# Kernel tuning notes

Hardware: AMD Instinct MI355X
Metric: run time of the kernel (lower is better)

The kernel has to match this reference:

```python
import jax, jax.numpy as jnp
import numpy as np

BN_EPS = 1e-5
K = 9  # 3x3 kernel positions


def conv2d(x, w, b, pad, dil=1):
    out = jax.lax.conv_general_dilated(
        x, w, window_strides=(1, 1), padding=((pad, pad), (pad, pad)),
        rhs_dilation=(dil, dil), dimension_numbers=('NCHW', 'OIHW', 'NCHW'))
    return out + b[None, :, None, None]


def bn_relu(x, g, be, mu, var):
    inv = jax.lax.rsqrt(var + BN_EPS)
    return jax.nn.relu((x - mu[None, :, None, None]) * (g * inv)[None, :, None, None] + be[None, :, None, None])


def deform_conv(x, w_om, b_om, w, b):
    # DCNv2-style modulated deformable 3x3 conv, stride 1, pad 1, dg=1.
    B, C, H, W = x.shape
    om = conv2d(x, w_om, b_om, pad=1)               # [B, 27, H, W]
    o1, o2, m = jnp.split(om, 3, axis=1)            # dy, dx, mask logits: [B,9,H,W]
    mask = jax.nn.sigmoid(m)
    ky, kx = jnp.meshgrid(jnp.arange(3), jnp.arange(3), indexing='ij')
    ky = (ky.reshape(-1) - 1).astype(x.dtype)       # kernel offsets in {-1,0,1}
    kx = (kx.reshape(-1) - 1).astype(x.dtype)
    py = jnp.arange(H, dtype=x.dtype)[None, None, :, None] + ky[None, :, None, None] + o1  # [B,9,H,W]
    px = jnp.arange(W, dtype=x.dtype)[None, None, None, :] + kx[None, :, None, None] + o2

    y0 = jnp.floor(py); x0 = jnp.floor(px)
    wy1 = py - y0; wx1 = px - x0
    y0i = y0.astype(jnp.int32); x0i = x0.astype(jnp.int32)
    x_flat = x.reshape(B, C, H * W)

    def corner(yi, xi, wgt):
        valid = ((yi >= 0) & (yi < H) & (xi >= 0) & (xi < W)).astype(x.dtype)
        idx = jnp.clip(yi, 0, H - 1) * W + jnp.clip(xi, 0, W - 1)      # [B,9,H,W]
        g = jax.vmap(lambda xf, i: xf[:, i])(x_flat, idx.reshape(B, -1))
        g = g.reshape(B, C, K, H, W)
        return g * (wgt * valid)[:, None]

    cols = (corner(y0i,     x0i,     (1 - wy1) * (1 - wx1))
            + corner(y0i,     x0i + 1, (1 - wy1) * wx1)
            + corner(y0i + 1, x0i,     wy1 * (1 - wx1))
            + corner(y0i + 1, x0i + 1, wy1 * wx1))                       # [B,C,9,H,W]
    cols = cols * mask[:, None]
    out = jnp.einsum('bckhw,ock->bohw', cols, w.reshape(w.shape[0], C, K))
    return out + b[None, :, None, None]


def setup_inputs() -> dict:
    key = jax.random.key(0)
    ks = jax.random.split(key, 24)
    B, C, H, W = 2, 64, 256, 256
    d = {}
    d['x'] = jax.random.normal(ks[0], (B, C, H, W), jnp.float32)
    d['w_om'] = jax.random.normal(ks[1], (27, C, 3, 3), jnp.float32) * 0.01
    d['b_om'] = jax.random.normal(ks[2], (27,), jnp.float32) * 0.01
    d['w_dcn'] = jax.random.normal(ks[3], (C, C, 3, 3), jnp.float32) * 0.05
    d['b_dcn'] = jax.random.normal(ks[4], (C,), jnp.float32) * 0.05
    for i, pfx in enumerate(['bn1', 'bn2', 'bn3']):
        d[pfx + '_g'] = jax.random.uniform(ks[5 + 4 * i], (C,), jnp.float32, 0.5, 1.5)
        d[pfx + '_b'] = jax.random.normal(ks[6 + 4 * i], (C,), jnp.float32) * 0.05
        d[pfx + '_m'] = jax.random.normal(ks[7 + 4 * i], (C,), jnp.float32) * 0.05
        d[pfx + '_v'] = jax.random.uniform(ks[8 + 4 * i], (C,), jnp.float32, 0.5, 1.5)
    d['w_h'] = jax.random.normal(ks[17], (C, C, 3, 3), jnp.float32) * 0.05
    d['b_h'] = jax.random.normal(ks[18], (C,), jnp.float32) * 0.05
    d['w_w'] = jax.random.normal(ks[19], (C, C, 3, 3), jnp.float32) * 0.05
    d['b_w'] = jax.random.normal(ks[20], (C,), jnp.float32) * 0.05
    d['w3'] = jax.random.normal(ks[21], (1, C, 3, 3), jnp.float32) * 0.05
    d['b3'] = jax.random.normal(ks[22], (1,), jnp.float32) * 0.05
    return d


def reference(x, w_om, b_om, w_dcn, b_dcn,
              bn1_g, bn1_b, bn1_m, bn1_v,
              w_h, b_h, bn2_g, bn2_b, bn2_m, bn2_v,
              w_w, b_w, bn3_g, bn3_b, bn3_m, bn3_v,
              w3, b3):
    h = deform_conv(x, w_om, b_om, w_dcn, b_dcn)
    h = bn_relu(h, bn1_g, bn1_b, bn1_m, bn1_v)
    h = conv2d(h, w_h, b_h, pad=2, dil=2)
    h = bn_relu(h, bn2_g, bn2_b, bn2_m, bn2_v)
    h = conv2d(h, w_w, b_w, pad=2, dil=2)
    h = bn_relu(h, bn3_g, bn3_b, bn3_m, bn3_v)
    h = conv2d(h, w3, b3, pad=1)
    return jnp.clip(jax.nn.sigmoid(h), 1e-4, 1.0 - 1e-4)
```

## Files before the change

kernel.cpp:

```cpp
#include <hip/hip_runtime.h>
#include <math.h>

#define HH 256
#define WW 256
#define HW (HH*WW)
#define NPX (2*HW)

typedef __attribute__((ext_vector_type(8))) short bf16x8;
typedef __attribute__((ext_vector_type(4))) float f32x4;

__device__ __forceinline__ float bf2f(short h) {
    union { unsigned u; float f; } v; v.u = ((unsigned)(unsigned short)h) << 16; return v.f;
}
__device__ __forceinline__ short f2bf(float f) {
    union { float f; unsigned u; } v; v.f = f;
    unsigned r = v.u + 0x7fffu + ((v.u >> 16) & 1u);
    return (short)(r >> 16);
}
__device__ __forceinline__ short f2bf_fast(float f) {
    union { float f; unsigned u; } v; v.f = f;
    return (short)((v.u + 0x8000u) >> 16);
}

__global__ __launch_bounds__(256) void k_prep_w(
        const float* __restrict__ w_om, const float* __restrict__ w_dcn,
        const float* __restrict__ w_h,  const float* __restrict__ w_w,
        const float* __restrict__ w3,
        short* __restrict__ wt_om, short* __restrict__ wt_dcn,
        short* __restrict__ wt_h,  short* __restrict__ wt_w,
        float* __restrict__ w3t) {
    int i = blockIdx.x * 256 + threadIdx.x;
    if (i >= 64 * 576) return;
    int o = i / 576, k = i - o * 576, t = k >> 6, c = k & 63;
    int kb = k >> 3, j = k & 7;
    int src = (o * 64 + c) * 9 + t;
    int dst = (kb * 64 + o) * 8 + j;
    wt_dcn[dst] = f2bf(w_dcn[src]);
    wt_h[dst]   = f2bf(w_h[src]);
    wt_w[dst]   = f2bf(w_w[src]);
    if (o < 32) wt_om[(kb * 32 + o) * 8 + j] = (o < 27) ? f2bf(w_om[src]) : (short)0;
    if (o == 0) w3t[k] = w3[c * 9 + t];
}

__global__ __launch_bounds__(256) void k_x2cl(const float* __restrict__ x,
        short* __restrict__ xcl) {
    __shared__ short tile[256 * 66];
    const int xx = threadIdx.x;
    const int row = blockIdx.x;
    const int b = row >> 8, y = row & 255;
    for (int c = 0; c < 64; ++c)
        tile[xx * 66 + c] = f2bf(x[((b * 64 + c) << 16) + (y << 8) + xx]);
    __syncthreads();
    short* op = xcl + ((row << 8) + xx) * 64;
#pragma unroll
    for (int j = 0; j < 8; ++j) {
        bf16x8 v;
#pragma unroll
        for (int e = 0; e < 8; ++e) v[e] = tile[xx * 66 + j * 8 + e];
        *(bf16x8*)(op + j * 8) = v;
    }
}

#define XPS 72

__global__ __launch_bounds__(256) __attribute__((amdgpu_waves_per_eu(2, 4)))
void k_dcn_mfma(const short* __restrict__ xcl,
        const short* __restrict__ wom, const float* __restrict__ b_om,
        const short* __restrict__ wt,
        const float* __restrict__ bias,
        const float* __restrict__ gg, const float* __restrict__ be,
        const float* __restrict__ mu, const float* __restrict__ var,
        short* __restrict__ out_cl) {
    __shared__ short xt[256 * XPS];
    __shared__ float om_lds[64 * 28];
    const int lane = threadIdx.x & 63, wave = threadIdx.x >> 6;
    const int quad = lane >> 4, l16 = lane & 15;
    const int band = blockIdx.x & 7, idx = blockIdx.x >> 3;
    const int tr = band * 8 + (idx >> 5), tc = idx & 31;
    const int b = tr >> 5;
    const int ty0 = (tr & 31) * 8, tx0 = tc * 8;
    const int base = b << 16;
    const int hy0 = ty0 - 4, hx0 = tx0 - 4;
    {
        const int p = threadIdx.x;
        const int sy = min(max(hy0 + (p >> 4), 0), 255);
        const int sx = min(max(hx0 + (p & 15), 0), 255);
        const short* src = xcl + (size_t)((base + sy * 256 + sx) * 64);
        short* dst = &xt[p * XPS];
#pragma unroll
        for (int j = 0; j < 8; ++j)
            *(bf16x8*)(dst + j * 8) = *(const bf16x8*)(src + j * 8);
    }
    __syncthreads();

    const int lp = wave * 16 + l16;
    const int pyy = lp >> 3, pxx = lp & 7;
    const int y = ty0 + pyy, x = tx0 + pxx;

    {
        f32x4 oacc[2];
        oacc[0] = (f32x4){0,0,0,0}; oacc[1] = (f32x4){0,0,0,0};
        auto loadOB = [&](int s, bf16x8* Bv) {
            const int kb = s * 4 + quad;
#pragma unroll
            for (int g = 0; g < 2; ++g)
                Bv[g] = *(const bf16x8*)(wom + (kb * 32 + g * 16 + l16) * 8);
        };
        bf16x8 OB[2][2];
        loadOB(0, OB[0]);
#pragma unroll
        for (int s = 0; s < 18; ++s) {
            if (s < 17) loadOB(s + 1, OB[(s + 1) & 1]);
            const int t = s >> 1, c0 = (s & 1) * 32;
            const int dy = t / 3 - 1, dx = t % 3 - 1;
            bf16x8 av = *(const bf16x8*)&xt[((pyy + 4 + dy) * 16 + (pxx + 4 + dx)) * XPS + c0 + quad * 8];
            bool ok = ((unsigned)(y + dy) < 256u) && ((unsigned)(x + dx) < 256u);
            if (!ok) { bf16x8 z = {0,0,0,0,0,0,0,0}; av = z; }
#pragma unroll
            for (int g = 0; g < 2; ++g)
                oacc[g] = __builtin_amdgcn_mfma_f32_16x16x32_bf16(av, OB[s & 1][g], oacc[g], 0, 0, 0);
        }
#pragma unroll
        for (int g = 0; g < 2; ++g) {
            int o = g * 16 + l16;
            if (o < 27) {
                float bo = b_om[o];
#pragma unroll
                for (int r = 0; r < 4; ++r) {
                    float v = oacc[g][r] + bo;
                    if (o >= 18) v = 1.f / (1.f + expf(-v));
                    om_lds[(wave * 16 + quad * 4 + r) * 28 + o] = v;
                }
            }
        }
    }
    __syncthreads();

    f32x4 acc[4];
#pragma unroll
    for (int i = 0; i < 4; ++i) acc[i] = (f32x4){0,0,0,0};

    const f32x4* omv4 = (const f32x4*)&om_lds[lp * 28];
    float omr[27];
#pragma unroll
    for (int i = 0; i < 7; ++i) {
        f32x4 v = omv4[i];
#pragma unroll
        for (int e = 0; e < 4; ++e) { int j = i * 4 + e; if (j < 27) omr[j] = v[e]; }
    }

#pragma unroll
    for (int t = 0; t < 9; ++t) {
        const int ky = t / 3 - 1, kx = t % 3 - 1;
        float o1 = omr[t], o2 = omr[9 + t], m = omr[18 + t];
        float py = (float)(y + ky) + o1;
        float px = (float)(x + kx) + o2;
        float y0f = floorf(py), x0f = floorf(px);
        float wy1 = py - y0f, wx1 = px - x0f;
        int y0 = (int)y0f, xi0 = (int)x0f, y1 = y0 + 1, xi1 = xi0 + 1;
        float w00 = (1.f - wy1) * (1.f - wx1) * m;
        float w01 = (1.f - wy1) * wx1 * m;
        float w10 = wy1 * (1.f - wx1) * m;
        float w11 = wy1 * wx1 * m;
        if (!((unsigned)y0  < 256u)) { w00 = 0.f; w01 = 0.f; }
        if (!((unsigned)y1  < 256u)) { w10 = 0.f; w11 = 0.f; }
        if (!((unsigned)xi0 < 256u)) { w00 = 0.f; w10 = 0.f; }
        if (!((unsigned)xi1 < 256u)) { w01 = 0.f; w11 = 0.f; }
        int cy0 = min(max(y0, 0), 255), cy1 = min(max(y1, 0), 255);
        int cx0 = min(max(xi0, 0), 255), cx1 = min(max(xi1, 0), 255);
        int iy0 = cy0 - hy0, iy1 = cy1 - hy0;
        int ix0 = cx0 - hx0, ix1 = cx1 - hx0;
        bool inh = ((unsigned)iy0 < 16u) && ((unsigned)iy1 < 16u)
                && ((unsigned)ix0 < 16u) && ((unsigned)ix1 < 16u);

        bf16x8 C[2][4];
        if (__all(inh)) {
            const int p00 = (iy0 * 16 + ix0) * XPS, p01 = (iy0 * 16 + ix1) * XPS;
            const int p10 = (iy1 * 16 + ix0) * XPS, p11 = (iy1 * 16 + ix1) * XPS;
#pragma unroll
            for (int h = 0; h < 2; ++h) {
                const int cb = h * 32 + quad * 8;
                C[h][0] = *(const bf16x8*)&xt[p00 + cb];
                C[h][1] = *(const bf16x8*)&xt[p01 + cb];
                C[h][2] = *(const bf16x8*)&xt[p10 + cb];
                C[h][3] = *(const bf16x8*)&xt[p11 + cb];
            }
        } else {
            const int i00 = (base + cy0 * 256 + cx0) * 64;
            const int i01 = (base + cy0 * 256 + cx1) * 64;
            const int i10 = (base + cy1 * 256 + cx0) * 64;
            const int i11 = (base + cy1 * 256 + cx1) * 64;
#pragma unroll
            for (int h = 0; h < 2; ++h) {
                const int cb = h * 32 + quad * 8;
                C[h][0] = *(const bf16x8*)(xcl + i00 + cb);
                C[h][1] = *(const bf16x8*)(xcl + i01 + cb);
                C[h][2] = *(const bf16x8*)(xcl + i10 + cb);
                C[h][3] = *(const bf16x8*)(xcl + i11 + cb);
            }
        }
#pragma unroll
        for (int h = 0; h < 2; ++h) {
            bf16x8 av;
#pragma unroll
            for (int e = 0; e < 8; ++e) {
                float s = w00 * bf2f(C[h][0][e]) + w01 * bf2f(C[h][1][e])
                        + w10 * bf2f(C[h][2][e]) + w11 * bf2f(C[h][3][e]);
                av[e] = f2bf_fast(s);
            }
            const int kb = t * 8 + h * 4 + quad;
#pragma unroll
            for (int g = 0; g < 4; ++g) {
                bf16x8 bv = *(const bf16x8*)(wt + (kb * 64 + g * 16 + l16) * 8);
                acc[g] = __builtin_amdgcn_mfma_f32_16x16x32_bf16(av, bv, acc[g], 0, 0, 0);
            }
        }
    }
#pragma unroll
    for (int g = 0; g < 4; ++g) {
        int o = g * 16 + l16;
        float sc = gg[o] * rsqrtf(var[o] + 1e-5f);
        float off = (bias[o] - mu[o]) * sc + be[o];
#pragma unroll
        for (int r = 0; r < 4; ++r) {
            int mm = quad * 4 + r;
            int pix = base + ((ty0 + wave * 2 + (mm >> 3)) << 8) + tx0 + (mm & 7);
            float v = acc[g][r] * sc + off;
            out_cl[(size_t)pix * 64 + o] = f2bf(fmaxf(v, 0.f));
        }
    }
}

__global__ __launch_bounds__(256) __attribute__((amdgpu_waves_per_eu(2, 4)))
void k_conv_mfma(const short* __restrict__ in_cl,
        const short* __restrict__ wt, const float* __restrict__ bias,
        const float* __restrict__ gg, const float* __restrict__ be,
        const float* __restrict__ mu, const float* __restrict__ var,
        short* __restrict__ out_cl) {
    __shared__ short xt[240 * XPS];
    const int lane = threadIdx.x & 63, wave = threadIdx.x >> 6;
    const int quad = lane >> 4, l16 = lane & 15;
    const int tIdx = (blockIdx.x & 7) * 128 + (blockIdx.x >> 3);
    const int tr = tIdx >> 4, tc = tIdx & 15;
    const int b = tr >> 5;
    const int ty0 = (tr & 31) * 8, tx0 = tc * 16;
    const int base = b << 16;
    if (threadIdx.x < 240) {
        const int p = threadIdx.x;
        const int sy = ty0 - 2 + p / 20, sx = tx0 - 2 + p % 20;
        short* dst = &xt[p * XPS];
        if (((unsigned)sy < 256u) && ((unsigned)sx < 256u)) {
            const short* src = in_cl + (size_t)((base + sy * 256 + sx) * 64);
#pragma unroll
            for (int j = 0; j < 8; ++j)
                *(bf16x8*)(dst + j * 8) = *(const bf16x8*)(src + j * 8);
        } else {
            bf16x8 z = {0,0,0,0,0,0,0,0};
#pragma unroll
            for (int j = 0; j < 8; ++j) *(bf16x8*)(dst + j * 8) = z;
        }
    }
    __syncthreads();
    const int ly = wave * 2;
    f32x4 acc[2][4];
#pragma unroll
    for (int h = 0; h < 2; ++h)
#pragma unroll
        for (int g = 0; g < 4; ++g) acc[h][g] = (f32x4){0,0,0,0};

    auto loadB = [&](int s, bf16x8* Bv) {
        const int kb = s * 4 + quad;
#pragma unroll
        for (int g = 0; g < 4; ++g)
            Bv[g] = *(const bf16x8*)(wt + (kb * 64 + g * 16 + l16) * 8);
    };
    bf16x8 B[3][4];
    loadB(0, B[0]);
    loadB(1, B[1]);
#pragma unroll
    for (int s = 0; s < 18; ++s) {
        if (s + 2 < 18) loadB(s + 2, B[(s + 2) % 3]);
        const int t = s >> 1, c0 = (s & 1) * 32;
        const int dy = (t / 3 - 1) * 2, dx = (t % 3 - 1) * 2;
        const int cidx = c0 + quad * 8;
        bf16x8 a0 = *(const bf16x8*)&xt[((ly + 2 + dy) * 20 + (l16 + 2 + dx)) * XPS + cidx];
        bf16x8 a1 = *(const bf16x8*)&xt[((ly + 3 + dy) * 20 + (l16 + 2 + dx)) * XPS + cidx];
#pragma unroll
        for (int g = 0; g < 4; ++g) {
            acc[0][g] = __builtin_amdgcn_mfma_f32_16x16x32_bf16(a0, B[s % 3][g], acc[0][g], 0, 0, 0);
            acc[1][g] = __builtin_amdgcn_mfma_f32_16x16x32_bf16(a1, B[s % 3][g], acc[1][g], 0, 0, 0);
        }
    }
#pragma unroll
    for (int h = 0; h < 2; ++h)
#pragma unroll
    for (int g = 0; g < 4; ++g) {
        int o = g * 16 + l16;
        float sc = gg[o] * rsqrtf(var[o] + 1e-5f);
        float off = (bias[o] - mu[o]) * sc + be[o];
#pragma unroll
        for (int r = 0; r < 4; ++r) {
            int pix = base + ((ty0 + ly + h) << 8) + tx0 + quad * 4 + r;
            float v = acc[h][g][r] * sc + off;
            out_cl[(size_t)pix * 64 + o] = f2bf(fmaxf(v, 0.f));
        }
    }
}

__global__ __launch_bounds__(256) void k_final(const short* __restrict__ h_cl,
        const float* __restrict__ w3t, const float* __restrict__ b3,
        float* __restrict__ out) {
    __shared__ short xt[324 * XPS];
    const int tIdx = (blockIdx.x & 7) * 64 + (blockIdx.x >> 3);
    const int tr = tIdx >> 4, tc = tIdx & 15;
    const int b = tr >> 4;
    const int ty0 = (tr & 15) * 16, tx0 = tc * 16;
    const int base = b << 16;
    for (int p = threadIdx.x; p < 324; p += 256) {
        const int sy = ty0 - 1 + p / 18, sx = tx0 - 1 + p % 18;
        short* dst = &xt[p * XPS];
        if (((unsigned)sy < 256u) && ((unsigned)sx < 256u)) {
            const short* src = h_cl + (size_t)((base + sy * 256 + sx) * 64);
#pragma unroll
            for (int j = 0; j < 8; ++j)
                *(bf16x8*)(dst + j * 8) = *(const bf16x8*)(src + j * 8);
        } else {
            bf16x8 z = {0,0,0,0,0,0,0,0};
#pragma unroll
            for (int j = 0; j < 8; ++j) *(bf16x8*)(dst + j * 8) = z;
        }
    }
    __syncthreads();
    const int ly = threadIdx.x >> 4, lx = threadIdx.x & 15;
    float acc = 0.f;
#pragma unroll
    for (int t = 0; t < 9; ++t) {
        const int hidx = (ly + 1 + t / 3 - 1) * 18 + (lx + 1 + t % 3 - 1);
        const short* hp = &xt[hidx * XPS];
        const float* wp = w3t + t * 64;
#pragma unroll
        for (int j = 0; j < 64; j += 8) {
            bf16x8 v = *(const bf16x8*)(hp + j);
#pragma unroll
            for (int e = 0; e < 8; ++e)
                acc = fmaf(bf2f(v[e]), wp[j + e], acc);
        }
    }
    float s = 1.f / (1.f + expf(-(acc + b3[0])));
    out[base + ((ty0 + ly) << 8) + tx0 + lx] = fminf(fmaxf(s, 1e-4f), 1.f - 1e-4f);
}

extern "C" void kernel_launch(void* const* d_in, const int* in_sizes, int n_in,
                              void* d_out, int out_size, void* d_ws, size_t ws_size,
                              hipStream_t stream) {
    const float* x     = (const float*)d_in[0];
    const float* w_om  = (const float*)d_in[1];
    const float* b_om  = (const float*)d_in[2];
    const float* w_dcn = (const float*)d_in[3];
    const float* b_dcn = (const float*)d_in[4];
    const float* bn1g = (const float*)d_in[5],  *bn1b = (const float*)d_in[6];
    const float* bn1m = (const float*)d_in[7],  *bn1v = (const float*)d_in[8];
    const float* bn2g = (const float*)d_in[9],  *bn2b = (const float*)d_in[10];
    const float* bn2m = (const float*)d_in[11], *bn2v = (const float*)d_in[12];
    const float* bn3g = (const float*)d_in[13], *bn3b = (const float*)d_in[14];
    const float* bn3m = (const float*)d_in[15], *bn3v = (const float*)d_in[16];
    const float* w_h = (const float*)d_in[17], *b_h = (const float*)d_in[18];
    const float* w_w = (const float*)d_in[19], *b_w = (const float*)d_in[20];
    const float* w3  = (const float*)d_in[21], *b3  = (const float*)d_in[22];
    float* outp = (float*)d_out;

    char* ws = (char*)d_ws;
    short* xcl   = (short*)ws;
    short* h1    = xcl + (size_t)NPX * 64;
    short* h2    = h1 + (size_t)NPX * 64;
    short* wt_om  = h2 + (size_t)NPX * 64;
    short* wt_dcn = wt_om  + 32 * 576;
    short* wt_h   = wt_dcn + 64 * 576;
    short* wt_w   = wt_h   + 64 * 576;
    float* w3t    = (float*)(wt_w + 64 * 576);

    dim3 blk(256);
    k_prep_w<<<(64 * 576 + 255) / 256, blk, 0, stream>>>(
        w_om, w_dcn, w_h, w_w, w3, wt_om, wt_dcn, wt_h, wt_w, w3t);
    k_x2cl<<<512, blk, 0, stream>>>(x, xcl);
    k_dcn_mfma<<<NPX / 64, blk, 0, stream>>>(xcl, wt_om, b_om, wt_dcn, b_dcn,
                                             bn1g, bn1b, bn1m, bn1v, h1);
    k_conv_mfma<<<NPX / 128, blk, 0, stream>>>(h1, wt_h, b_h, bn2g, bn2b, bn2m, bn2v, h2);
    k_conv_mfma<<<NPX / 128, blk, 0, stream>>>(h2, wt_w, b_w, bn3g, bn3b, bn3m, bn3v, h1);
    k_final<<<512, blk, 0, stream>>>(h1, w3t, b3, outp);
}
```

Before: 220.1 us.

## Pack bilinear interpolation into paired FMAs and enlarge dilated-conv tiles to 16x16

The deformable-conv bilinear blend now unpacks bf16 pairs into float2 vectors, uses packed FMAs and repacks with a byte-permute, which cuts the scalar conversion and ALU work per sample. The dilated conv kernels now run 512-thread blocks over 16x16 output tiles with a 20x20 halo in LDS. This lowers the halo overhead per output pixel and halves the block count to 512. The trade-offs are more LDS per block, which may reduce occupancy, and the new tile indexing must match the rest of the kernel body, which is not shown.

```diff
diff --git a/kernel.cpp b/kernel.cpp
--- a/kernel.cpp
+++ b/kernel.cpp
@@ -8,6 +8,7 @@
 
 typedef __attribute__((ext_vector_type(8))) short bf16x8;
 typedef __attribute__((ext_vector_type(4))) float f32x4;
+typedef __attribute__((ext_vector_type(2))) float f32x2;
 
 __device__ __forceinline__ float bf2f(short h) {
     union { unsigned u; float f; } v; v.u = ((unsigned)(unsigned short)h) << 16; return v.f;
@@ -17,9 +18,14 @@
     unsigned r = v.u + 0x7fffu + ((v.u >> 16) & 1u);
     return (short)(r >> 16);
 }
-__device__ __forceinline__ short f2bf_fast(float f) {
-    union { float f; unsigned u; } v; v.f = f;
-    return (short)((v.u + 0x8000u) >> 16);
+__device__ __forceinline__ float uasf(unsigned u) {
+    union { unsigned u; float f; } v; v.u = u; return v.f;
+}
+__device__ __forceinline__ unsigned fasu(float f) {
+    union { float f; unsigned u; } v; v.f = f; return v.u;
+}
+__device__ __forceinline__ f32x2 bfpair(unsigned u) {
+    f32x2 r; r[0] = uasf(u << 16); r[1] = uasf(u & 0xffff0000u); return r;
 }
 
 __global__ __launch_bounds__(256) void k_prep_w(
@@ -199,15 +205,26 @@
                 C[h][3] = *(const bf16x8*)(xcl + i11 + cb);
             }
         }
+        const f32x2 W00 = {w00, w00}, W01 = {w01, w01};
+        const f32x2 W10 = {w10, w10}, W11 = {w11, w11};
 #pragma unroll
         for (int h = 0; h < 2; ++h) {
-            bf16x8 av;
-#pragma unroll
-            for (int e = 0; e < 8; ++e) {
-                float s = w00 * bf2f(C[h][0][e]) + w01 * bf2f(C[h][1][e])
-                        + w10 * bf2f(C[h][2][e]) + w11 * bf2f(C[h][3][e]);
-                av[e] = f2bf_fast(s);
+            const unsigned* u0 = (const unsigned*)&C[h][0];
+            const unsigned* u1 = (const unsigned*)&C[h][1];
+            const unsigned* u2 = (const unsigned*)&C[h][2];
+            const unsigned* u3 = (const unsigned*)&C[h][3];
+            unsigned avu[4];
+#pragma unroll
+            for (int d = 0; d < 4; ++d) {
+                f32x2 s = bfpair(u0[d]) * W00;
+                s = __builtin_elementwise_fma(bfpair(u1[d]), W01, s);
+                s = __builtin_elementwise_fma(bfpair(u2[d]), W10, s);
+                s = __builtin_elementwise_fma(bfpair(u3[d]), W11, s);
+                unsigned r0 = fasu(s[0]) + 0x8000u;
+                unsigned r1 = fasu(s[1]) + 0x8000u;
+                avu[d] = __builtin_amdgcn_perm(r1, r0, 0x07060302u);
             }
+            bf16x8 av = *(const bf16x8*)avu;
             const int kb = t * 8 + h * 4 + quad;
 #pragma unroll
             for (int g = 0; g < 4; ++g) {
@@ -231,21 +248,21 @@
     }
 }
 
-__global__ __launch_bounds__(256) __attribute__((amdgpu_waves_per_eu(2, 4)))
+__global__ __launch_bounds__(512) __attribute__((amdgpu_waves_per_eu(2, 4)))
 void k_conv_mfma(const short* __restrict__ in_cl,
         const short* __restrict__ wt, const float* __restrict__ bias,
         const float* __restrict__ gg, const float* __restrict__ be,
         const float* __restrict__ mu, const float* __restrict__ var,
         short* __restrict__ out_cl) {
-    __shared__ short xt[240 * XPS];
+    __shared__ short xt[400 * XPS];
     const int lane = threadIdx.x & 63, wave = threadIdx.x >> 6;
     const int quad = lane >> 4, l16 = lane & 15;
-    const int tIdx = (blockIdx.x & 7) * 128 + (blockIdx.x >> 3);
+    const int tIdx = (blockIdx.x & 7) * 64 + (blockIdx.x >> 3);
     const int tr = tIdx >> 4, tc = tIdx & 15;
-    const int b = tr >> 5;
-    const int ty0 = (tr & 31) * 8, tx0 = tc * 16;
+    const int b = tr >> 4;
+    const int ty0 = (tr & 15) * 16, tx0 = tc * 16;
     const int base = b << 16;
-    if (threadIdx.x < 240) {
+    if (threadIdx.x < 400) {
         const int p = threadIdx.x;
         const int sy = ty0 - 2 + p / 20, sx = tx0 - 2 + p % 20;
         short* dst = &xt[p * XPS];
@@ -385,7 +402,7 @@
     k_x2cl<<<512, blk, 0, stream>>>(x, xcl);
     k_dcn_mfma<<<NPX / 64, blk, 0, stream>>>(xcl, wt_om, b_om, wt_dcn, b_dcn,
                                              bn1g, bn1b, bn1m, bn1v, h1);
-    k_conv_mfma<<<NPX / 128, blk, 0, stream>>>(h1, wt_h, b_h, bn2g, bn2b, bn2m, bn2v, h2);
-    k_conv_mfma<<<NPX / 128, blk, 0, stream>>>(h2, wt_w, b_w, bn3g, bn3b, bn3m, bn3v, h1);
+    k_conv_mfma<<<512, dim3(512), 0, stream>>>(h1, wt_h, b_h, bn2g, bn2b, bn2m, bn2v, h2);
+    k_conv_mfma<<<512, dim3(512), 0, stream>>>(h2, wt_w, b_w, bn3g, bn3b, bn3m, bn3v, h1);
     k_final<<<512, blk, 0, stream>>>(h1, w3t, b3, outp);
 }
```

Result: no change. 222.5 us (+1.1%).
